# Optimization experiments

Measured on AMD Instinct MI355X. Metric: run time of the kernel, lower is better.

The kernel has to match this reference:

```python
import jax, jax.numpy as jnp
import numpy as np

HIDDEN = 512

def setup_inputs() -> dict:
    key = jax.random.key(0)
    kx, kq, kk, kv = jax.random.split(key, 4)
    B, S, H = 4, 4096, HIDDEN
    scale = 1.0 / np.sqrt(H)
    x = jax.random.normal(kx, (B, S, H), dtype=jnp.float32)
    # nn.Linear weights are [out, in]; y = x @ W.T
    Wq = jax.random.normal(kq, (H, H), dtype=jnp.float32) * scale
    Wk = jax.random.normal(kk, (H, H), dtype=jnp.float32) * scale
    Wv = jax.random.normal(kv, (H, H), dtype=jnp.float32) * scale
    return {"x": x, "Wq": Wq, "Wk": Wk, "Wv": Wv}

def reference(x, Wq, Wk, Wv):
    H = x.shape[-1]
    q = jnp.einsum('bsh,oh->bso', x, Wq)
    k = jnp.einsum('bsh,oh->bso', x, Wk)
    v = jnp.einsum('bsh,oh->bso', x, Wv)
    scores = jnp.einsum('bqh,bkh->bqk', q, k) / jnp.sqrt(jnp.asarray(H, x.dtype))
    att = jax.nn.softmax(scores, axis=-1)  # max-subtracted softmax, same math as manual version
    return jnp.einsum('bqk,bkh->bqh', att, v)
```

## Files before the change

### kernel.cpp

```cpp
#include <hip/hip_runtime.h>
#include <stdint.h>

typedef unsigned short u16;
typedef __bf16  bf16x8   __attribute__((ext_vector_type(8)));
typedef float   floatx4  __attribute__((ext_vector_type(4)));
typedef unsigned short ushortx4 __attribute__((ext_vector_type(4)));

__device__ __forceinline__ u16 f2bf(float f) {
  unsigned u = __builtin_bit_cast(unsigned, f);
  u += 0x7FFFu + ((u >> 16) & 1u);
  return (u16)(u >> 16);
}

#define GLD_LDS16(g, l)                                                        \
  __builtin_amdgcn_global_load_lds(                                            \
      (const __attribute__((address_space(1))) void*)(g),                      \
      (__attribute__((address_space(3))) void*)(l), 16, 0, 0)

#define VMW(N) asm volatile("s_waitcnt vmcnt(" #N ")" ::: "memory")

__global__ __launch_bounds__(256) void cvt_w(
    const float* __restrict__ Wq, const float* __restrict__ Wk,
    const float* __restrict__ Wv, u16* __restrict__ dst)
{
  const int z = blockIdx.y;
  const float* src = (z == 0) ? Wq : (z == 1) ? Wk : Wv;
  u16* d = dst + (size_t)z * 262144;
  const int idx = (blockIdx.x * 256 + threadIdx.x) * 8;
  const float4 lo = *(const float4*)&src[idx];
  const float4 hi = *(const float4*)&src[idx + 4];
  union { u16 h[8]; uint4 v; } pk;
  pk.h[0] = f2bf(lo.x); pk.h[1] = f2bf(lo.y); pk.h[2] = f2bf(lo.z); pk.h[3] = f2bf(lo.w);
  pk.h[4] = f2bf(hi.x); pk.h[5] = f2bf(hi.y); pk.h[6] = f2bf(hi.z); pk.h[7] = f2bf(hi.w);
  *(uint4*)&d[idx] = pk.v;
}

__global__ __launch_bounds__(256) void cvt_x(
    const float* __restrict__ X, u16* __restrict__ dst)
{
  const int idx = (blockIdx.x * 256 + threadIdx.x) * 8;
  const float4 lo = *(const float4*)&X[idx];
  const float4 hi = *(const float4*)&X[idx + 4];
  union { u16 h[8]; uint4 v; } pk;
  pk.h[0] = f2bf(lo.x); pk.h[1] = f2bf(lo.y); pk.h[2] = f2bf(lo.z); pk.h[3] = f2bf(lo.w);
  pk.h[4] = f2bf(hi.x); pk.h[5] = f2bf(hi.y); pk.h[6] = f2bf(hi.z); pk.h[7] = f2bf(hi.w);
  *(uint4*)&dst[idx] = pk.v;
}

__global__ __launch_bounds__(256, 2) void qkv_gemm(
    const u16* __restrict__ X16, const u16* __restrict__ Wb,
    u16* __restrict__ qo, u16* __restrict__ ko, u16* __restrict__ vto)
{
  __shared__ u16 As[128 * 32];
  __shared__ u16 Bs[128 * 32];

  const int tid = threadIdx.x;
  const int w  = tid >> 6, l = tid & 63;
  const int lr = l & 15, lq = l >> 4;
  const int lk = lq * 8;
  const int m0 = blockIdx.x * 128;
  const int n0 = blockIdx.y * 128;
  const int z  = blockIdx.z;
  const u16* W = Wb + (size_t)z * 262144;
  const int wm = (w & 1) * 64, wn = (w >> 1) * 64;

  floatx4 acc[4][4];
  const floatx4 fz = {0.f, 0.f, 0.f, 0.f};
#pragma unroll
  for (int i = 0; i < 4; ++i)
#pragma unroll
    for (int j = 0; j < 4; ++j) acc[i][j] = fz;

  for (int kk = 0; kk < 512; kk += 32) {
    __syncthreads();
#pragma unroll
    for (int i = 0; i < 2; ++i) {
      const int c = i * 256 + tid;
      const int row = c >> 2, c8 = (c & 3) * 8;
      GLD_LDS16(X16 + (size_t)(m0 + row) * 512 + kk + c8, &As[c * 8]);
      GLD_LDS16(W   + (size_t)(n0 + row) * 512 + kk + c8, &Bs[c * 8]);
    }
    __syncthreads();

    bf16x8 af[4], bfr[4];
#pragma unroll
    for (int t = 0; t < 4; ++t) {
      af[t]  = *(const bf16x8*)&As[(wm + t * 16 + lr) * 32 + lk];
      bfr[t] = *(const bf16x8*)&Bs[(wn + t * 16 + lr) * 32 + lk];
    }
#pragma unroll
    for (int i = 0; i < 4; ++i)
#pragma unroll
      for (int j = 0; j < 4; ++j)
        acc[i][j] = __builtin_amdgcn_mfma_f32_16x16x32_bf16(af[i], bfr[j],
                                                            acc[i][j], 0, 0, 0);
  }

  const int cr = lq * 4;
  if (z == 2) {
#pragma unroll
    for (int i = 0; i < 4; ++i)
#pragma unroll
      for (int j = 0; j < 4; ++j) {
        const int n = n0 + wn + j * 16 + lr;
        const int m = m0 + wm + i * 16 + cr;
        ushortx4 pk;
#pragma unroll
        for (int r = 0; r < 4; ++r) pk[r] = f2bf(acc[i][j][r]);
        *(ushortx4*)&vto[(size_t)n * 16384 + m] = pk;
      }
  } else {
    u16* dst = (z == 0) ? qo : ko;
    const float sc = (z == 0) ? 0.06375871732f : 1.0f;
#pragma unroll
    for (int i = 0; i < 4; ++i)
#pragma unroll
      for (int j = 0; j < 4; ++j) {
        const int m = m0 + wm + i * 16 + cr;
        const int n = n0 + wn + j * 16 + lr;
#pragma unroll
        for (int r = 0; r < 4; ++r)
          dst[(size_t)(m + r) * 512 + n] = f2bf(acc[i][j][r] * sc);
      }
  }
}

__global__ __launch_bounds__(512, 2) void qk_exp8(
    const u16* __restrict__ q, const u16* __restrict__ k,
    u16* __restrict__ S, float* __restrict__ lsum)
{
  __shared__ u16 lds[65536];

  const int tid = threadIdx.x;
  const int w  = tid >> 6, l = tid & 63;
  const int lr = l & 15, lq = l >> 4;
  const int wA = (w & 1) * 16;
  const int wB = (w >> 1) * 16;
  const int kb0 = blockIdx.x * 256;
  const int qb0 = blockIdx.y * 256;
  const int b   = blockIdx.z;
  const size_t rb = (size_t)b * 4096;
  const u16* kg = k + rb * 512;
  const u16* qg = q + rb * 512;

  floatx4 acc[8][4];
  const floatx4 fz = {0.f, 0.f, 0.f, 0.f};
#pragma unroll
  for (int i = 0; i < 8; ++i)
#pragma unroll
    for (int j = 0; j < 4; ++j) acc[i][j] = fz;

  auto stage = [&](int s) {
    const int ts = s >> 2, kind = s & 3;
    const int mat = kind & 1, h = kind >> 1;
    const u16* src = mat ? qg : kg;
    const int rbase = mat ? qb0 : kb0;
    u16* dst = &lds[(ts & 1) * 32768 + mat * 16384];
#pragma unroll
    for (int i = 0; i < 2; ++i) {
      const int c = i * 512 + tid;
      const int r = h * 128 + (c >> 3), k16 = c & 7;
      const int k16s = k16 ^ (r & 7);
      GLD_LDS16(src + (size_t)(rbase + r) * 512 + ts * 64 + k16s * 8,
                &dst[r * 64 + k16 * 8]);
    }
  };

#pragma unroll
  for (int s = 0; s < 6; ++s) stage(s);
  VMW(4);
  __builtin_amdgcn_s_barrier();
  __builtin_amdgcn_sched_barrier(0);

  bf16x8 af[4][2];
  bf16x8 bf0[2][2], bf1[2][2];

#pragma unroll
  for (int t = 0; t < 8; ++t) {
#pragma unroll
    for (int qd = 0; qd < 4; ++qd) {
      const int fmh = qd >> 1;
      const int fnh = fmh ^ (qd & 1);
      const u16* AB = &lds[(t & 1) * 32768];
      const u16* BB = AB + 16384;

      if (qd == 0 || qd == 2) {
#pragma unroll
        for (int im = 0; im < 4; ++im) {
          const int rA = (fmh * 4 + im) * 32 + wA + lr;
#pragma unroll
          for (int ks = 0; ks < 2; ++ks) {
            const int k16p = (ks * 4 + lq) ^ (rA & 7);
            af[im][ks] = *(const bf16x8*)&AB[rA * 64 + k16p * 8];
          }
        }
      }
      if (qd == 0) {
#pragma unroll
        for (int jn = 0; jn < 2; ++jn) {
          const int rB = jn * 64 + wB + lr;
#pragma unroll
          for (int ks = 0; ks < 2; ++ks) {
            const int k16p = (ks * 4 + lq) ^ (rB & 7);
            bf0[jn][ks] = *(const bf16x8*)&BB[rB * 64 + k16p * 8];
          }
        }
      }
      if (qd == 1) {
#pragma unroll
        for (int jn = 0; jn < 2; ++jn) {
          const int rB = (2 + jn) * 64 + wB + lr;
#pragma unroll
          for (int ks = 0; ks < 2; ++ks) {
            const int k16p = (ks * 4 + lq) ^ (rB & 7);
            bf1[jn][ks] = *(const bf16x8*)&BB[rB * 64 + k16p * 8];
          }
        }
      }

      const int s = t * 4 + qd + 6;
      if (s < 32) stage(s);

      __builtin_amdgcn_sched_barrier(0);
      __builtin_amdgcn_s_barrier();
      asm volatile("s_waitcnt lgkmcnt(0)" ::: "memory");
      __builtin_amdgcn_sched_barrier(0);

      __builtin_amdgcn_s_setprio(1);
      if (fnh) {
#pragma unroll
        for (int im = 0; im < 4; ++im)
#pragma unroll
          for (int jn = 0; jn < 2; ++jn)
#pragma unroll
            for (int ks = 0; ks < 2; ++ks)
              acc[fmh * 4 + im][2 + jn] =
                  __builtin_amdgcn_mfma_f32_16x16x32_bf16(
                      af[im][ks], bf1[jn][ks], acc[fmh * 4 + im][2 + jn], 0, 0, 0);
      } else {
#pragma unroll
        for (int im = 0; im < 4; ++im)
#pragma unroll
          for (int jn = 0; jn < 2; ++jn)
#pragma unroll
            for (int ks = 0; ks < 2; ++ks)
              acc[fmh * 4 + im][jn] =
                  __builtin_amdgcn_mfma_f32_16x16x32_bf16(
                      af[im][ks], bf0[jn][ks], acc[fmh * 4 + im][jn], 0, 0, 0);
      }
      __builtin_amdgcn_s_setprio(0);

      if (qd == 3) {
        if (t < 6)        VMW(4);
        else if (t == 6)  VMW(0);
      }
      __builtin_amdgcn_s_barrier();
      __builtin_amdgcn_sched_barrier(0);
    }
  }

  const int cr = lq * 4;
  u16* Sb = S + ((size_t)b << 24);
  float js[4] = {0.f, 0.f, 0.f, 0.f};
#pragma unroll
  for (int fm = 0; fm < 8; ++fm)
#pragma unroll
    for (int fn = 0; fn < 4; ++fn) {
      const int key = kb0 + fm * 32 + wA + cr;
      const int qr  = qb0 + fn * 64 + wB + lr;
      ushortx4 pk;
      float s4 = 0.f;
#pragma unroll
      for (int r = 0; r < 4; ++r) {
        const float p = __builtin_amdgcn_exp2f(acc[fm][fn][r] - 17.31234049f);
        s4 += p;
        pk[r] = f2bf(p);
      }
      js[fn] += s4;
      *(ushortx4*)&Sb[(size_t)qr * 4096 + key] = pk;
    }
#pragma unroll
  for (int fn = 0; fn < 4; ++fn) {
    float s = js[fn];
    s += __shfl_xor(s, 16);
    s += __shfl_xor(s, 32);
    if (lq == 0)
      atomicAdd(&lsum[rb + qb0 + fn * 64 + wB + lr], s);
  }
}

#define PV_STG_A(TT, CK) do {                                                  \
    u16* dA_ = &lds[((TT) & 1) * 24576];                                       \
    _Pragma("unroll")                                                          \
    for (int i_ = 0; i_ < 2; ++i_) {                                           \
      const int c_ = i_ * 512 + tid, r_ = c_ >> 3, k_ = c_ & 7;                \
      GLD_LDS16(Sb + (size_t)(lm0 + (CK) * 128 + r_) * 4096 + (TT) * 64 +      \
                    (k_ ^ (r_ & 7)) * 8,                                       \
                &dA_[((CK) * 128 + r_) * 64 + k_ * 8]);                        \
    }                                                                          \
  } while (0)

#define PV_STG_B(TT) do {                                                      \
    u16* dB_ = &lds[((TT) & 1) * 24576 + 16384];                               \
    _Pragma("unroll")                                                          \
    for (int i_ = 0; i_ < 2; ++i_) {                                           \
      const int c_ = i_ * 512 + tid, r_ = c_ >> 3, k_ = c_ & 7;                \
      GLD_LDS16(vt + (size_t)(n0 + r_) * 16384 + bofs + (TT) * 64 +            \
                    (k_ ^ (r_ & 7)) * 8,                                       \
                &dB_[r_ * 64 + k_ * 8]);                                       \
    }                                                                          \
  } while (0)

#define PV_PH(T, PH, STAGE_CODE, TAIL_CODE) do {                               \
    const u16* AB_ = &lds[((T) & 1) * 24576];                                  \
    const u16* BB_ = AB_ + 16384;                                              \
    _Pragma("unroll")                                                          \
    for (int im_ = 0; im_ < 4; ++im_) {                                        \
      const int rA_ = ((PH) * 4 + im_) * 32 + wm16 + lr;                       \
      _Pragma("unroll")                                                        \
      for (int ks_ = 0; ks_ < 2; ++ks_) {                                      \
        const int kp_ = (ks_ * 4 + lq) ^ (rA_ & 7);                            \
        af[im_][ks_] = *(const bf16x8*)&AB_[rA_ * 64 + kp_ * 8];               \
      }                                                                        \
    }                                                                          \
    if ((PH) == 0) {                                                           \
      _Pragma("unroll")                                                        \
      for (int jn_ = 0; jn_ < 2; ++jn_) {                                      \
        const int rB_ = wn32 + jn_ * 16 + lr;                                  \
        _Pragma("unroll")                                                      \
        for (int ks_ = 0; ks_ < 2; ++ks_) {                                    \
          const int kp_ = (ks_ * 4 + lq) ^ (rB_ & 7);                          \
          bfv[jn_][ks_] = *(const bf16x8*)&BB_[rB_ * 64 + kp_ * 8];            \
        }                                                                      \
      }                                                                        \
    }                                                                          \
    STAGE_CODE;                                                                \
    __builtin_amdgcn_sched_barrier(0);                                         \
    __builtin_amdgcn_s_barrier();                                              \
    asm volatile("s_waitcnt lgkmcnt(0)" ::: "memory");                         \
    __builtin_amdgcn_sched_barrier(0);                                         \
    __builtin_amdgcn_s_setprio(1);                                             \
    _Pragma("unroll")                                                          \
    for (int im_ = 0; im_ < 4; ++im_)                                          \
      _Pragma("unroll")                                                        \
      for (int jn_ = 0; jn_ < 2; ++jn_)                                        \
        _Pragma("unroll")                                                      \
        for (int ks_ = 0; ks_ < 2; ++ks_)                                      \
          acc[(PH) * 4 + im_][jn_] = __builtin_amdgcn_mfma_f32_16x16x32_bf16(  \
              af[im_][ks_], bfv[jn_][ks_], acc[(PH) * 4 + im_][jn_], 0, 0, 0); \
    __builtin_amdgcn_s_setprio(0);                                             \
    TAIL_CODE;                                                                 \
    __builtin_amdgcn_s_barrier();                                              \
    __builtin_amdgcn_sched_barrier(0);                                         \
  } while (0)

#define PV_TILE(T, G_A1, G_A0B, VMCODE) do {                                   \
    PV_PH(T, 0, { if (G_A1) PV_STG_A((T) + 1, 1); }, (void)0);                 \
    PV_PH(T, 1, { if (G_A0B) { PV_STG_A((T) + 2, 0); PV_STG_B((T) + 2); } },   \
          VMCODE);                                                             \
  } while (0)

__global__ __launch_bounds__(512, 2) void pv8(
    const u16* __restrict__ S, const u16* __restrict__ vt,
    const float* __restrict__ lsum, float* __restrict__ out)
{
  __shared__ u16 lds[49152];

  const int tid = threadIdx.x;
  const int w  = tid >> 6, l = tid & 63;
  const int lr = l & 15, lq = l >> 4;
  const int wm16 = (w & 1) * 16;
  const int wn32 = (w >> 1) * 32;

  const int wg = blockIdx.x;
  const int li = (wg & 7) * 32 + (wg >> 3);
  const int n0 = (li & 3) * 128;
  const int m0 = (li >> 2) * 256;
  const int b  = m0 >> 12;
  const int lm0 = m0 & 4095;
  const u16* Sb = S + ((size_t)b << 24);
  const size_t bofs = (size_t)b * 4096;

  floatx4 acc[8][2];
  const floatx4 fz = {0.f, 0.f, 0.f, 0.f};
#pragma unroll
  for (int i = 0; i < 8; ++i) { acc[i][0] = fz; acc[i][1] = fz; }

  bf16x8 af[4][2], bfv[2][2];

  PV_STG_A(0, 0); PV_STG_B(0); PV_STG_A(0, 1); PV_STG_A(1, 0); PV_STG_B(1);
  VMW(4);
  __builtin_amdgcn_s_barrier();
  __builtin_amdgcn_sched_barrier(0);

  for (int t = 0; t < 62; t += 2) {
    PV_TILE(t,     1, 1, VMW(4));
    PV_TILE(t + 1, 1, 1, VMW(4));
  }
  PV_TILE(62, 1, 0, VMW(0));
  PV_TILE(63, 0, 0, (void)0);

  const int cr = lq * 4;
#pragma unroll
  for (int fm = 0; fm < 8; ++fm) {
    const int m = m0 + fm * 32 + wm16 + cr;
    float inv[4];
#pragma unroll
    for (int r = 0; r < 4; ++r) inv[r] = 1.0f / lsum[m + r];
#pragma unroll
    for (int jn = 0; jn < 2; ++jn) {
      const int n = n0 + wn32 + jn * 16 + lr;
#pragma unroll
      for (int r = 0; r < 4; ++r)
        out[(size_t)(m + r) * 512 + n] = acc[fm][jn][r] * inv[r];
    }
  }
}

extern "C" void kernel_launch(void* const* d_in, const int* in_sizes, int n_in,
                              void* d_out, int out_size, void* d_ws, size_t ws_size,
                              hipStream_t stream) {
  (void)in_sizes; (void)n_in; (void)out_size; (void)ws_size;
  const float* x  = (const float*)d_in[0];
  const float* Wq = (const float*)d_in[1];
  const float* Wk = (const float*)d_in[2];
  const float* Wv = (const float*)d_in[3];
  float* out = (float*)d_out;
  u16* ws  = (u16*)d_ws;
  u16* qw  = ws;
  u16* kw  = qw + (size_t)16384 * 512;
  u16* vw  = kw + (size_t)16384 * 512;
  u16* x16 = vw + (size_t)16384 * 512;
  u16* wb  = x16 + (size_t)16384 * 512;
  u16* Sp  = wb + (size_t)3 * 262144;
  float* lsum = (float*)(Sp + ((size_t)4 << 24));

  hipMemsetAsync(lsum, 0, 16384 * sizeof(float), stream);
  cvt_w<<<dim3(128, 3), dim3(256), 0, stream>>>(Wq, Wk, Wv, wb);
  cvt_x<<<dim3(4096), dim3(256), 0, stream>>>(x, x16);
  qkv_gemm<<<dim3(128, 4, 3), dim3(256), 0, stream>>>(x16, wb, qw, kw, vw);
  qk_exp8<<<dim3(16, 16, 4), dim3(512), 0, stream>>>(qw, kw, Sp, lsum);
  pv8<<<dim3(256), dim3(512), 0, stream>>>(Sp, vw, lsum, out);
}
```

Measured before the change: 291.0 us.

## Rewrite QKV projection GEMM as 256x256-tile pipelined kernel with swizzled LDS

Replaces the 128x128 two-barrier QKV GEMM with a 512-thread kernel computing 256x256 tiles. It streams K=64 slices into double-buffered, XOR-swizzled LDS via async global-to-LDS loads issued several stages ahead, interleaved with MFMA phases and priority hints. For Q and K it swaps operands so results are stored transposed-coalesced into row-major output. A 1D grid remaps blocks across XCDs. The aim is to hide load latency, cut LDS bank conflicts and raise data reuse per tile, at the cost of more registers and fewer blocks (384).

New measurement: 279.6 us. 3.9% less time.

```diff
diff --git a/kernel.cpp b/kernel.cpp
--- a/kernel.cpp
+++ b/kernel.cpp
@@ -47,82 +47,161 @@
   *(uint4*)&dst[idx] = pk.v;
 }
 
-__global__ __launch_bounds__(256, 2) void qkv_gemm(
+__global__ __launch_bounds__(512, 2) void qkv8(
     const u16* __restrict__ X16, const u16* __restrict__ Wb,
     u16* __restrict__ qo, u16* __restrict__ ko, u16* __restrict__ vto)
 {
-  __shared__ u16 As[128 * 32];
-  __shared__ u16 Bs[128 * 32];
+  __shared__ u16 lds[65536];
 
   const int tid = threadIdx.x;
   const int w  = tid >> 6, l = tid & 63;
   const int lr = l & 15, lq = l >> 4;
-  const int lk = lq * 8;
-  const int m0 = blockIdx.x * 128;
-  const int n0 = blockIdx.y * 128;
-  const int z  = blockIdx.z;
-  const u16* W = Wb + (size_t)z * 262144;
-  const int wm = (w & 1) * 64, wn = (w >> 1) * 64;
-
-  floatx4 acc[4][4];
+  const int wA = (w & 1) * 16;
+  const int wB = (w >> 1) * 16;
+
+  const int bx = blockIdx.x;
+  const int li = (bx & 7) * 48 + (bx >> 3);
+  const int z  = li >> 7, u = li & 127;
+
+  const u16* Ag; const u16* Bg; u16* dst; float sc; size_t ostr; int mb, nb;
+  if (z < 2) {
+    Ag = Wb + (size_t)z * 262144; Bg = X16;
+    dst = z ? ko : qo; sc = z ? 1.0f : 0.06375871732f; ostr = 512;
+    mb = (u & 1) * 256;  nb = (u >> 1) * 256;
+  } else {
+    Ag = X16; Bg = Wb + (size_t)2 * 262144;
+    dst = vto; sc = 1.0f; ostr = 16384;
+    mb = (u >> 1) * 256; nb = (u & 1) * 256;
+  }
+
+  floatx4 acc[8][4];
   const floatx4 fz = {0.f, 0.f, 0.f, 0.f};
 #pragma unroll
-  for (int i = 0; i < 4; ++i)
+  for (int i = 0; i < 8; ++i)
 #pragma unroll
     for (int j = 0; j < 4; ++j) acc[i][j] = fz;
 
-  for (int kk = 0; kk < 512; kk += 32) {
-    __syncthreads();
+  auto stage = [&](int s) {
+    const int ts = s >> 2, kind = s & 3;
+    const int mat = kind & 1, h = kind >> 1;
+    const u16* src = mat ? Bg : Ag;
+    const int rbase = mat ? nb : mb;
+    u16* dstl = &lds[(ts & 1) * 32768 + mat * 16384];
 #pragma unroll
     for (int i = 0; i < 2; ++i) {
-      const int c = i * 256 + tid;
-      const int row = c >> 2, c8 = (c & 3) * 8;
-      GLD_LDS16(X16 + (size_t)(m0 + row) * 512 + kk + c8, &As[c * 8]);
-      GLD_LDS16(W   + (size_t)(n0 + row) * 512 + kk + c8, &Bs[c * 8]);
-    }
-    __syncthreads();
-
-    bf16x8 af[4], bfr[4];
-#pragma unroll
-    for (int t = 0; t < 4; ++t) {
-      af[t]  = *(const bf16x8*)&As[(wm + t * 16 + lr) * 32 + lk];
-      bfr[t] = *(const bf16x8*)&Bs[(wn + t * 16 + lr) * 32 + lk];
-    }
-#pragma unroll
-    for (int i = 0; i < 4; ++i)
-#pragma unroll
-      for (int j = 0; j < 4; ++j)
-        acc[i][j] = __builtin_amdgcn_mfma_f32_16x16x32_bf16(af[i], bfr[j],
-                                                            acc[i][j], 0, 0, 0);
+      const int c = i * 512 + tid;
+      const int r = h * 128 + (c >> 3), k16 = c & 7;
+      const int k16s = k16 ^ (r & 7);
+      GLD_LDS16(src + (size_t)(rbase + r) * 512 + ts * 64 + k16s * 8,
+                &dstl[r * 64 + k16 * 8]);
+    }
+  };
+
+#pragma unroll
+  for (int s = 0; s < 6; ++s) stage(s);
+  VMW(4);
+  __builtin_amdgcn_s_barrier();
+  __builtin_amdgcn_sched_barrier(0);
+
+  bf16x8 af[4][2];
+  bf16x8 bf0[2][2], bf1[2][2];
+
+#pragma unroll
+  for (int t = 0; t < 8; ++t) {
+#pragma unroll
+    for (int qd = 0; qd < 4; ++qd) {
+      const int fmh = qd >> 1;
+      const int fnh = fmh ^ (qd & 1);
+      const u16* AB = &lds[(t & 1) * 32768];
+      const u16* BB = AB + 16384;
+
+      if (qd == 0 || qd == 2) {
+#pragma unroll
+        for (int im = 0; im < 4; ++im) {
+          const int rA = (fmh * 4 + im) * 32 + wA + lr;
+#pragma unroll
+          for (int ks = 0; ks < 2; ++ks) {
+            const int k16p = (ks * 4 + lq) ^ (rA & 7);
+            af[im][ks] = *(const bf16x8*)&AB[rA * 64 + k16p * 8];
+          }
+        }
+      }
+      if (qd == 0) {
+#pragma unroll
+        for (int jn = 0; jn < 2; ++jn) {
+          const int rB = jn * 64 + wB + lr;
+#pragma unroll
+          for (int ks = 0; ks < 2; ++ks) {
+            const int k16p = (ks * 4 + lq) ^ (rB & 7);
+            bf0[jn][ks] = *(const bf16x8*)&BB[rB * 64 + k16p * 8];
+          }
+        }
+      }
+      if (qd == 1) {
+#pragma unroll
+        for (int jn = 0; jn < 2; ++jn) {
+          const int rB = (2 + jn) * 64 + wB + lr;
+#pragma unroll
+          for (int ks = 0; ks < 2; ++ks) {
+            const int k16p = (ks * 4 + lq) ^ (rB & 7);
+            bf1[jn][ks] = *(const bf16x8*)&BB[rB * 64 + k16p * 8];
+          }
+        }
+      }
+
+      const int s = t * 4 + qd + 6;
+      if (s < 32) stage(s);
+
+      __builtin_amdgcn_sched_barrier(0);
+      __builtin_amdgcn_s_barrier();
+      asm volatile("s_waitcnt lgkmcnt(0)" ::: "memory");
+      __builtin_amdgcn_sched_barrier(0);
+
+      __builtin_amdgcn_s_setprio(1);
+      if (fnh) {
+#pragma unroll
+        for (int im = 0; im < 4; ++im)
+#pragma unroll
+          for (int jn = 0; jn < 2; ++jn)
+#pragma unroll
+            for (int ks = 0; ks < 2; ++ks)
+              acc[fmh * 4 + im][2 + jn] =
+                  __builtin_amdgcn_mfma_f32_16x16x32_bf16(
+                      af[im][ks], bf1[jn][ks], acc[fmh * 4 + im][2 + jn], 0, 0, 0);
+      } else {
+#pragma unroll
+        for (int im = 0; im < 4; ++im)
+#pragma unroll
+          for (int jn = 0; jn < 2; ++jn)
+#pragma unroll
+            for (int ks = 0; ks < 2; ++ks)
+              acc[fmh * 4 + im][jn] =
+                  __builtin_amdgcn_mfma_f32_16x16x32_bf16(
+                      af[im][ks], bf0[jn][ks], acc[fmh * 4 + im][jn], 0, 0, 0);
+      }
+      __builtin_amdgcn_s_setprio(0);
+
+      if (qd == 3) {
+        if (t < 6)        VMW(4);
+        else if (t == 6)  VMW(0);
+      }
+      __builtin_amdgcn_s_barrier();
+      __builtin_amdgcn_sched_barrier(0);
+    }
   }
 
   const int cr = lq * 4;
-  if (z == 2) {
-#pragma unroll
-    for (int i = 0; i < 4; ++i)
-#pragma unroll
-      for (int j = 0; j < 4; ++j) {
-        const int n = n0 + wn + j * 16 + lr;
-        const int m = m0 + wm + i * 16 + cr;
-        ushortx4 pk;
-#pragma unroll
-        for (int r = 0; r < 4; ++r) pk[r] = f2bf(acc[i][j][r]);
-        *(ushortx4*)&vto[(size_t)n * 16384 + m] = pk;
-      }
-  } else {
-    u16* dst = (z == 0) ? qo : ko;
-    const float sc = (z == 0) ? 0.06375871732f : 1.0f;
-#pragma unroll
-    for (int i = 0; i < 4; ++i)
-#pragma unroll
-      for (int j = 0; j < 4; ++j) {
-        const int m = m0 + wm + i * 16 + cr;
-        const int n = n0 + wn + j * 16 + lr;
-#pragma unroll
-        for (int r = 0; r < 4; ++r)
-          dst[(size_t)(m + r) * 512 + n] = f2bf(acc[i][j][r] * sc);
-      }
-  }
+#pragma unroll
+  for (int fm = 0; fm < 8; ++fm)
+#pragma unroll
+    for (int fn = 0; fn < 4; ++fn) {
+      const int mv = mb + fm * 32 + wA + cr;
+      const int nv = nb + fn * 64 + wB + lr;
+      ushortx4 pk;
+#pragma unroll
+      for (int r = 0; r < 4; ++r) pk[r] = f2bf(acc[fm][fn][r] * sc);
+      *(ushortx4*)&dst[(size_t)nv * ostr + mv] = pk;
+    }
 }
 
 __global__ __launch_bounds__(512, 2) void qk_exp8(
@@ -438,7 +517,7 @@
   hipMemsetAsync(lsum, 0, 16384 * sizeof(float), stream);
   cvt_w<<<dim3(128, 3), dim3(256), 0, stream>>>(Wq, Wk, Wv, wb);
   cvt_x<<<dim3(4096), dim3(256), 0, stream>>>(x, x16);
-  qkv_gemm<<<dim3(128, 4, 3), dim3(256), 0, stream>>>(x16, wb, qw, kw, vw);
+  qkv8<<<dim3(384), dim3(512), 0, stream>>>(x16, wb, qw, kw, vw);
   qk_exp8<<<dim3(16, 16, 4), dim3(512), 0, stream>>>(qw, kw, Sp, lsum);
   pv8<<<dim3(256), dim3(512), 0, stream>>>(Sp, vw, lsum, out);
 }
```
